# Performance work log

Hardware: AMD Instinct MI355X
Metric: run time of the kernel (lower is better)

Reference implementation:

```python
import jax, jax.numpy as jnp
import numpy as np

DEPTH = 4
CHUNK = 16


def tp(a, b):
    """Graded tensor (outer) product on flattened levels: (...,m)x(...,n)->(...,m*n)."""
    return jnp.einsum('...i,...j->...ij', a, b).reshape(*a.shape[:-1], a.shape[-1] * b.shape[-1])


def ta_mul(a, b):
    """Truncated tensor-algebra product of two group-like elements (implicit level-0 == 1).
    a, b: lists of levels 1..D, level k flattened to C**k."""
    out = []
    for k in range(len(a)):
        t = a[k] + b[k]
        for i in range(k):
            t = t + tp(a[i], b[k - 1 - i])
        out.append(t)
    return out


def ta_mulz(a, b):
    """Product when both elements have level-0 == 0."""
    out = []
    for k in range(len(a)):
        t = jnp.zeros_like(a[k])
        for i in range(k):
            t = t + tp(a[i], b[k - 1 - i])
        out.append(t)
    return out


def ta_exp(a):
    """exp of a level-0-free element, truncated at DEPTH; returns levels 1..D (level-0 == 1 implicit)."""
    out = list(a)
    p = a
    fact = 1.0
    for m in range(2, len(a) + 1):
        p = ta_mulz(a, p)
        fact *= m
        out = [o + q / fact for o, q in zip(out, p)]
    return out


def ta_log(s):
    """Truncated log of group-like element g = 1 + s; input s = levels 1..D of g."""
    out = list(s)
    p = s
    sign = 1.0
    for m in range(2, len(s) + 1):
        p = ta_mulz(s, p)
        sign = -sign
        out = [o + (sign / m) * q for o, q in zip(out, p)]
    return out


def bch(a, b):
    """BCH merge: log(exp(a) (x) exp(b)) in the truncated algebra."""
    return ta_log(ta_mul(ta_exp(a), ta_exp(b)))


def exp_l1(d):
    """exp of a pure level-1 element d (shape (...,C)): level k = d^(x)k / k!."""
    levels = [d]
    cur = d
    fact = 1.0
    for k in range(2, DEPTH + 1):
        cur = tp(cur, d)
        fact *= k
        levels.append(cur / fact)
    return levels


def chunk_signatures(inc):
    """inc: (B, N, L, C) per-chunk increments -> signature levels [(B,N,C), (B,N,C^2), ...]
    via Chen: sig = exp(d_1) (x) ... (x) exp(d_L)."""
    carry0 = tuple(exp_l1(inc[:, :, 0]))
    xs = jnp.moveaxis(inc[:, :, 1:], 2, 0)  # (L-1, B, N, C)
    def step(carry, d):
        return tuple(ta_mul(list(carry), exp_l1(d))), None
    carry, _ = jax.lax.scan(step, carry0, xs)
    return list(carry)


def hillis_steele(levels):
    """Inclusive associative scan over chunk dim (axis=1) with BCH merge.
    bch(0, b) == b exactly, so zero-padding handles the boundary."""
    N = levels[0].shape[1]
    pref = levels
    d = 1
    while d < N:
        shifted = [jnp.concatenate([jnp.zeros_like(l[:, :d]), l[:, :-d]], axis=1) for l in pref]
        pref = bch(shifted, pref)
        d *= 2
    return pref


def _forward(x, W1, b1, W2, b2):
    B, T, Cin = x.shape
    t = jnp.linspace(0.0, 1.0, T, dtype=x.dtype)
    path = jnp.concatenate([x, jnp.broadcast_to(t[None, :, None], (B, T, 1)).astype(x.dtype)], axis=-1)
    C = Cin + 1
    # basepoint=True: path starts at 0, so increments are diff of [0; path]
    inc = jnp.diff(path, axis=1, prepend=jnp.zeros((B, 1, C), x.dtype))
    N = T // CHUNK
    inc = inc.reshape(B, N, CHUNK, C)
    sig = chunk_signatures(inc)          # levels 1..D, (B,N,C^k)
    logl = ta_log(sig)                   # truncated log-signature per chunk
    pref = hillis_steele(logl)           # inclusive BCH prefix scan
    flat = jnp.concatenate(pref, axis=-1)  # (B, N, mem_dim)
    pooled = flat.mean(axis=1)           # readout_pool == 'mean'
    h = jnp.maximum(pooled @ W1 + b1, 0.0)
    return h @ W2 + b2


def setup_inputs() -> dict:
    key = jax.random.key(0)
    k0, k1, k2 = jax.random.split(key, 3)
    B, T, Cin = 8, 2048, 7
    mem_dim, H, out_dim = 4680, 256, 1
    x = jax.random.normal(k0, (B, T, Cin), dtype=jnp.float32)
    W1 = jax.random.normal(k1, (mem_dim, H), dtype=jnp.float32) * (1.0 / np.sqrt(mem_dim))
    b1 = jnp.zeros((H,), jnp.float32)
    W2 = jax.random.normal(k2, (H, out_dim), dtype=jnp.float32) * (1.0 / np.sqrt(H))
    b2 = jnp.zeros((out_dim,), jnp.float32)
    return {"x": x, "W1": W1, "b1": b1, "W2": W2, "b2": b2}


def reference(x, W1, b1, W2, b2):
    return _forward(x, W1, b1, W2, b2)
```

## Files before the change

### kernel.cpp

```cpp
#include <hip/hip_runtime.h>


#define MEM   4680
#define OFF2  8
#define OFF3  72
#define OFF4  584
#define NCH   128
#define NG    32
#define LCH   4
#define TLEN  2048
#define GSTR  20

__global__ __launch_bounds__(256) void group_sig_kernel(const float* __restrict__ x,
                                                        float* __restrict__ Q) {
    int blk = blockIdx.x;
    int b = blk >> 5, g = blk & 31;
    int tid = threadIdx.x;
    int lane = tid & 63, w = tid >> 6;
    int kq = lane >> 3, lq = lane & 7;

    __shared__ float sInc[64 * 8];
    __shared__ __attribute__((aligned(16))) float sG[512 * GSTR];
    __shared__ float sA[MEM];
    __shared__ float loc3[512];
    __shared__ float loc2[64];
    __shared__ float loc1[8];

    for (int e = tid; e < 64 * 8; e += 256) {
        int s = e >> 3, c = e & 7;
        int t = g * 64 + s;
        float v;
        if (c < 7) {
            float cur  = x[(b * TLEN + t) * 7 + c];
            float prev = (t > 0) ? x[(b * TLEN + t - 1) * 7 + c] : 0.0f;
            v = cur - prev;
        } else {
            v = (t > 0) ? (1.0f / 2047.0f) : 0.0f;
        }
        sInc[e] = v;
    }
    for (int m = tid; m < MEM; m += 256) sA[m] = 0.0f;
    __syncthreads();

    for (int c = 0; c < LCH; c++) {
        const float* dch = &sInc[c * 128];

        int pos1 = tid, pos2 = tid + 256;
        int i1 = pos1 >> 6, j1 = (pos1 >> 3) & 7, k1 = pos1 & 7;
        int i2 = pos2 >> 6;
        float p1a = 0.0f, l2a = 0.0f, l3a = 0.0f;
        float p1b = 0.0f, l2b = 0.0f, l3b = 0.0f;
        float ga[16], gb[16];
#pragma unroll
        for (int t = 0; t < 16; t++) {
            float di1 = dch[t * 8 + i1], di2 = dch[t * 8 + i2];
            float dj = dch[t * 8 + j1], dk = dch[t * 8 + k1];
            ga[t] = l3a + dk * (l2a * 0.5f + dj * (p1a * (1.0f / 6.0f) + di1 * (1.0f / 24.0f)));
            gb[t] = l3b + dk * (l2b * 0.5f + dj * (p1b * (1.0f / 6.0f) + di2 * (1.0f / 24.0f)));
            l3a += dk * (l2a + dj * (p1a * 0.5f + di1 * (1.0f / 6.0f)));
            l3b += dk * (l2b + dj * (p1b * 0.5f + di2 * (1.0f / 6.0f)));
            l2a += p1a * dj + di1 * dj * 0.5f;
            l2b += p1b * dj + di2 * dj * 0.5f;
            p1a += di1;
            p1b += di2;
        }
        {
            float4* gp1 = (float4*)&sG[pos1 * GSTR];
            float4* gp2 = (float4*)&sG[pos2 * GSTR];
            gp1[0] = make_float4(ga[0], ga[1], ga[2], ga[3]);
            gp1[1] = make_float4(ga[4], ga[5], ga[6], ga[7]);
            gp1[2] = make_float4(ga[8], ga[9], ga[10], ga[11]);
            gp1[3] = make_float4(ga[12], ga[13], ga[14], ga[15]);
            gp2[0] = make_float4(gb[0], gb[1], gb[2], gb[3]);
            gp2[1] = make_float4(gb[4], gb[5], gb[6], gb[7]);
            gp2[2] = make_float4(gb[8], gb[9], gb[10], gb[11]);
            gp2[3] = make_float4(gb[12], gb[13], gb[14], gb[15]);
        }
        loc3[pos1] = l3a;
        loc3[pos2] = l3b;
        if (k1 == 0) { loc2[pos1 >> 3] = l2a; loc2[pos2 >> 3] = l2b; }
        if ((pos1 & 63) == 0) { loc1[i1] = p1a; loc1[i2] = p1b; }
        __syncthreads();

        float dl[16];
#pragma unroll
        for (int t = 0; t < 16; t++) dl[t] = dch[t * 8 + lq];

        float r4[16];
#pragma unroll
        for (int r = 0; r < 16; r++) {
            int row = w + 4 * r;
            int i = row >> 3, j = row & 7;
            int m = row * 64 + lane;
            const float4* gp = (const float4*)&sG[(row * 8 + kq) * GSTR];
            float4 g0 = gp[0], g1 = gp[1], g2 = gp[2], g3 = gp[3];
            float acc = g0.x * dl[0] + g0.y * dl[1] + g0.z * dl[2] + g0.w * dl[3]
                      + g1.x * dl[4] + g1.y * dl[5] + g1.z * dl[6] + g1.w * dl[7]
                      + g2.x * dl[8] + g2.y * dl[9] + g2.z * dl[10] + g2.w * dl[11]
                      + g3.x * dl[12] + g3.y * dl[13] + g3.z * dl[14] + g3.w * dl[15];
            r4[r] = sA[OFF4 + m] + acc
                  + sA[i] * loc3[j * 64 + lane]
                  + sA[OFF2 + row] * loc2[lane]
                  + sA[OFF3 + row * 8 + kq] * loc1[lq];
        }
        float r3[2];
#pragma unroll
        for (int q = 0; q < 2; q++) {
            int m3 = tid + 256 * q;
            float l3v = (q == 0) ? l3a : l3b;
            r3[q] = sA[OFF3 + m3] + l3v
                  + sA[m3 >> 6] * loc2[m3 & 63]
                  + sA[OFF2 + (m3 >> 3)] * loc1[m3 & 7];
        }
        float r2v = 0.0f, r1v = 0.0f;
        if (tid < 64) r2v = sA[OFF2 + tid] + loc2[tid] + sA[tid >> 3] * loc1[tid & 7];
        if (tid < 8)  r1v = sA[tid] + loc1[tid];
        __syncthreads();

        size_t qbase = (size_t)(blk * LCH + c) * MEM;
#pragma unroll
        for (int r = 0; r < 16; r++) {
            int row = w + 4 * r;
            int m = row * 64 + lane;
            sA[OFF4 + m] = r4[r];
            Q[qbase + OFF4 + m] = r4[r];
        }
        sA[OFF3 + tid] = r3[0];       Q[qbase + OFF3 + tid] = r3[0];
        sA[OFF3 + 256 + tid] = r3[1]; Q[qbase + OFF3 + 256 + tid] = r3[1];
        if (tid < 64) { sA[OFF2 + tid] = r2v; Q[qbase + OFF2 + tid] = r2v; }
        if (tid < 8)  { sA[tid] = r1v;        Q[qbase + tid] = r1v; }
        __syncthreads();
    }
}

__global__ __launch_bounds__(256) void scan_low_kernel(const float* __restrict__ Q,
                                                       float* __restrict__ P) {
    int b = blockIdx.x;
    int tid = threadIdx.x;

    __shared__ float st1[NG][8];
    __shared__ float sp1[NG][8];
    __shared__ float st2[NG][64];
    __shared__ float sp2[NG][64];

    {
        int g = tid >> 3, i = tid & 7;
        st1[g][i] = Q[((size_t)((b * NG + g) * LCH + 3)) * MEM + i];
    }
    for (int m = tid; m < NG * 64; m += 256) {
        int g = m >> 6, e = m & 63;
        st2[g][e] = Q[((size_t)((b * NG + g) * LCH + 3)) * MEM + OFF2 + e];
    }
    __syncthreads();

    if (tid < 8) {
        float acc = 0.0f;
        for (int g = 0; g < NG; g++) { sp1[g][tid] = acc; acc += st1[g][tid]; }
    }
    __syncthreads();
    if (tid < 64) {
        int i = tid >> 3, k = tid & 7;
        float acc = 0.0f;
        for (int g = 0; g < NG; g++) {
            sp2[g][tid] = acc;
            acc += st2[g][tid] + sp1[g][i] * st1[g][k];
        }
    }
    __syncthreads();

    {
        int g = tid >> 3, i = tid & 7;
        P[(size_t)(b * NG + g) * MEM + i] = sp1[g][i];
    }
    for (int m = tid; m < NG * 64; m += 256) {
        int g = m >> 6, e = m & 63;
        P[(size_t)(b * NG + g) * MEM + OFF2 + e] = sp2[g][e];
    }

    int m1 = tid, m2 = tid + 256;
    int i1 = m1 >> 6, jk1 = m1 & 63, ij1 = m1 >> 3, k1 = m1 & 7;
    int i2 = m2 >> 6, jk2 = m2 & 63, ij2 = m2 >> 3, k2 = m2 & 7;
    float acc1 = 0.0f, acc2 = 0.0f;
#pragma unroll 4
    for (int g = 0; g < NG; g++) {
        size_t prow = (size_t)(b * NG + g) * MEM;
        size_t qrow = (size_t)((b * NG + g) * LCH + 3) * MEM;
        P[prow + OFF3 + m1] = acc1;
        P[prow + OFF3 + m2] = acc2;
        acc1 += Q[qrow + OFF3 + m1] + sp1[g][i1] * st2[g][jk1] + sp2[g][ij1] * st1[g][k1];
        acc2 += Q[qrow + OFF3 + m2] + sp1[g][i2] * st2[g][jk2] + sp2[g][ij2] * st1[g][k2];
    }
}

__global__ __launch_bounds__(256) void scan_l4_kernel(const float* __restrict__ Q,
                                                      float* __restrict__ P) {
    int bx = blockIdx.x;
    int b = bx >> 4, s = bx & 15;
    int m = s * 256 + threadIdx.x;
    int i = m >> 9, jkl = m & 511, ij = m >> 6, ijk = m >> 3, kl = m & 63, l = m & 7;

    float acc = 0.0f;
#pragma unroll 4
    for (int g = 0; g < NG; g++) {
        size_t prow = (size_t)(b * NG + g) * MEM;
        size_t qrow = (size_t)((b * NG + g) * LCH + 3) * MEM;
        P[prow + OFF4 + m] = acc;
        acc += Q[qrow + OFF4 + m]
             + P[prow + i] * Q[qrow + OFF3 + jkl]
             + P[prow + OFF2 + ij] * Q[qrow + OFF2 + kl]
             + P[prow + OFF3 + ijk] * Q[qrow + l];
    }
}

__global__ __launch_bounds__(256) void apply_log_pool_kernel(const float* __restrict__ Q,
                                                             const float* __restrict__ P,
                                                             float* __restrict__ pooled) {
    int blk = blockIdx.x;
    int b = blk >> 5;
    int tid = threadIdx.x;
    int lane = tid & 63, w = tid >> 6;
    int kq = lane >> 3, lq = lane & 7;

    __shared__ float sA[MEM];
    __shared__ float sB[MEM];
    __shared__ float sR[OFF4];
    __shared__ float sP23[512];

    {
        size_t pbase = (size_t)blk * MEM;
        const float4* src = (const float4*)(P + pbase);
        float4* dst = (float4*)sA;
        for (int m = tid; m < MEM / 4; m += 256) dst[m] = src[m];
    }

    float pool4[16];
#pragma unroll
    for (int r = 0; r < 16; r++) pool4[r] = 0.0f;
    float pool3[2] = {0.0f, 0.0f};
    float pool2 = 0.0f, pool1 = 0.0f;

    for (int c = 0; c < LCH; c++) {
        __syncthreads();
        {
            size_t baseQ = (size_t)(blk * LCH + c) * MEM;
            const float4* src = (const float4*)(Q + baseQ);
            float4* dst = (float4*)sB;
            for (int m = tid; m < MEM / 4; m += 256) dst[m] = src[m];
        }
        __syncthreads();

        float b1l = sB[lq];
        float b2lane = sB[OFF2 + lane];

        float r1 = 0.0f, r2v = 0.0f;
        float r3v[2];
#pragma unroll
        for (int q = 0; q < 2; q++) {
            int m3 = tid + 256 * q;
            r3v[q] = sA[OFF3 + m3] + sB[OFF3 + m3]
                   + sA[m3 >> 6] * sB[OFF2 + (m3 & 63)]
                   + sA[OFF2 + (m3 >> 3)] * sB[m3 & 7];
        }
        if (tid < 64) r2v = sA[OFF2 + tid] + sB[OFF2 + tid] + sA[tid >> 3] * sB[tid & 7];
        if (tid < 8)  r1 = sA[tid] + sB[tid];

        float r4[16];
#pragma unroll
        for (int r = 0; r < 16; r++) {
            int row = w + 4 * r;
            int i = row >> 3, j = row & 7;
            int m = row * 64 + lane;
            r4[r] = sA[OFF4 + m] + sB[OFF4 + m]
                  + sA[i] * sB[OFF3 + j * 64 + lane]
                  + sA[OFF2 + row] * b2lane
                  + sA[OFF3 + row * 8 + kq] * b1l;
        }

#pragma unroll
        for (int q = 0; q < 2; q++) sR[OFF3 + tid + 256 * q] = r3v[q];
        if (tid < 64) sR[OFF2 + tid] = r2v;
        if (tid < 8)  sR[tid] = r1;
        __syncthreads();

#pragma unroll
        for (int q = 0; q < 2; q++) {
            int m3 = tid + 256 * q;
            int i = m3 >> 6;
            sP23[m3] = sR[i] * sR[OFF2 + (m3 & 63)]
                     + sR[OFF2 + i * 8 + ((m3 >> 3) & 7)] * sR[m3 & 7];
        }
        __syncthreads();

        float s1l = sR[lq];
        float s2lane = sR[OFF2 + lane];
        float p22lane = sR[kq] * sR[lq];
#pragma unroll
        for (int r = 0; r < 16; r++) {
            int row = w + 4 * r;
            int i = row >> 3, j = row & 7;
            float s1i = sR[i];
            float p24 = s1i * sR[OFF3 + j * 64 + lane] + sR[OFF2 + row] * s2lane
                      + sR[OFF3 + row * 8 + kq] * s1l;
            float p34 = s1i * sP23[j * 64 + lane] + sR[OFF2 + row] * p22lane;
            float p44 = s1i * sR[j] * p22lane;
            pool4[r] += r4[r] - 0.5f * p24 + (1.0f / 3.0f) * p34 - 0.25f * p44;
        }
#pragma unroll
        for (int q = 0; q < 2; q++) {
            int m3 = tid + 256 * q;
            int i3 = m3 >> 6;
            pool3[q] += r3v[q] - 0.5f * sP23[m3] + (1.0f / 3.0f) * sR[i3] * p22lane;
        }
        if (tid < 64) pool2 += r2v - 0.5f * sR[tid >> 3] * sR[tid & 7];
        if (tid < 8)  pool1 += r1;
    }

    const float sc = 1.0f / (float)NCH;
    float* pb = pooled + (size_t)b * MEM;
#pragma unroll
    for (int r = 0; r < 16; r++) {
        int row = w + 4 * r;
        atomicAdd(&pb[OFF4 + row * 64 + lane], pool4[r] * sc);
    }
    atomicAdd(&pb[OFF3 + tid], pool3[0] * sc);
    atomicAdd(&pb[OFF3 + 256 + tid], pool3[1] * sc);
    if (tid < 64) atomicAdd(&pb[OFF2 + tid], pool2 * sc);
    if (tid < 8)  atomicAdd(&pb[tid], pool1 * sc);
}

#define ZN (8 * MEM + 8 * 256)
__global__ __launch_bounds__(256) void zero_kernel(float* __restrict__ buf) {
    int i = blockIdx.x * 256 + threadIdx.x;
    if (i < ZN) buf[i] = 0.0f;
}

__global__ __launch_bounds__(256) void gemv1_kernel(const float* __restrict__ pooled,
                                                    const float* __restrict__ W1,
                                                    float* __restrict__ hbuf) {
    int kc = blockIdx.x;
    int tid = threadIdx.x;
    int k0 = kc * 32;
    __shared__ float sp[8][32];
    {
        int b = tid >> 5, kk = tid & 31;
        sp[b][kk] = (k0 + kk < MEM) ? pooled[b * MEM + k0 + kk] : 0.0f;
    }
    __syncthreads();
    float acc[8];
#pragma unroll
    for (int b = 0; b < 8; b++) acc[b] = 0.0f;
    int kend = (k0 + 32 < MEM) ? (k0 + 32) : MEM;
    for (int k = k0; k < kend; k++) {
        float wv = W1[(size_t)k * 256 + tid];
#pragma unroll
        for (int b = 0; b < 8; b++) acc[b] += sp[b][k - k0] * wv;
    }
#pragma unroll
    for (int b = 0; b < 8; b++) atomicAdd(&hbuf[b * 256 + tid], acc[b]);
}

__global__ __launch_bounds__(256) void final_kernel(const float* __restrict__ hbuf,
                                                    const float* __restrict__ b1,
                                                    const float* __restrict__ W2,
                                                    const float* __restrict__ b2,
                                                    float* __restrict__ outp) {
    int b = blockIdx.x;
    int tid = threadIdx.x;
    float v = hbuf[b * 256 + tid] + b1[tid];
    v = fmaxf(v, 0.0f) * W2[tid];
    __shared__ float sRed[256];
    sRed[tid] = v;
    __syncthreads();
    for (int s = 128; s > 0; s >>= 1) {
        if (tid < s) sRed[tid] += sRed[tid + s];
        __syncthreads();
    }
    if (tid == 0) outp[b] = sRed[0] + b2[0];
}

extern "C" void kernel_launch(void* const* d_in, const int* in_sizes, int n_in,
                              void* d_out, int out_size, void* d_ws, size_t ws_size,
                              hipStream_t stream) {
    const float* x  = (const float*)d_in[0];
    const float* W1 = (const float*)d_in[1];
    const float* b1 = (const float*)d_in[2];
    const float* W2 = (const float*)d_in[3];
    const float* b2 = (const float*)d_in[4];
    float* out = (float*)d_out;

    float* ws = (float*)d_ws;
    float* Q      = ws;
    float* P      = Q + (size_t)1024 * MEM;
    float* pooled = P + (size_t)256 * MEM;
    float* hbuf   = pooled + 8 * MEM;

    zero_kernel<<<(ZN + 255) / 256, 256, 0, stream>>>(pooled);
    group_sig_kernel<<<256, 256, 0, stream>>>(x, Q);
    scan_low_kernel<<<8, 256, 0, stream>>>(Q, P);
    scan_l4_kernel<<<128, 256, 0, stream>>>(Q, P);
    apply_log_pool_kernel<<<256, 256, 0, stream>>>(Q, P, pooled);
    gemv1_kernel<<<147, 256, 0, stream>>>(pooled, W1, hbuf);
    final_kernel<<<8, 256, 0, stream>>>(hbuf, b1, W2, b2, out);
}
```

Baseline: 136.6 us.

## Fuse scan kernels, fold zeroing into group kernel, preload all chunks

Merges the low-level and level-4 prefix-scan kernels into one 128-block kernel. Each block recomputes the level-1/2 scans, computes its own slice of level-3, and keeps these prefixes in shared memory so the level-4 pass needs no global P reads. The zero kernel is folded into the group-signature kernel. The apply kernel now loads all four chunk Q rows into shared memory up front, which removes per-chunk syncs but makes shared memory much larger and lowers occupancy. Together these cut two kernel launches and a global round trip of prefix data.

```diff
diff --git a/kernel.cpp b/kernel.cpp
--- a/kernel.cpp
+++ b/kernel.cpp
@@ -10,14 +10,18 @@
 #define LCH   4
 #define TLEN  2048
 #define GSTR  20
+#define ZN    (8 * MEM + 8 * 256)
 
 __global__ __launch_bounds__(256) void group_sig_kernel(const float* __restrict__ x,
-                                                        float* __restrict__ Q) {
+                                                        float* __restrict__ Q,
+                                                        float* __restrict__ zbuf) {
     int blk = blockIdx.x;
     int b = blk >> 5, g = blk & 31;
     int tid = threadIdx.x;
     int lane = tid & 63, w = tid >> 6;
     int kq = lane >> 3, lq = lane & 7;
+
+    for (int i = blk * 256 + tid; i < ZN; i += 256 * 256) zbuf[i] = 0.0f;
 
     __shared__ float sInc[64 * 8];
     __shared__ __attribute__((aligned(16))) float sG[512 * GSTR];
@@ -133,15 +137,18 @@
     }
 }
 
-__global__ __launch_bounds__(256) void scan_low_kernel(const float* __restrict__ Q,
-                                                       float* __restrict__ P) {
-    int b = blockIdx.x;
+__global__ __launch_bounds__(256) void scan_fused_kernel(const float* __restrict__ Q,
+                                                         float* __restrict__ P) {
+    int bx = blockIdx.x;
+    int b = bx >> 4, s = bx & 15;
     int tid = threadIdx.x;
 
     __shared__ float st1[NG][8];
+    __shared__ float st2[NG][64];
+    __shared__ float st3[NG][32];
     __shared__ float sp1[NG][8];
-    __shared__ float st2[NG][64];
     __shared__ float sp2[NG][64];
+    __shared__ float sp3[NG][32];
 
     {
         int g = tid >> 3, i = tid & 7;
@@ -151,64 +158,53 @@
         int g = m >> 6, e = m & 63;
         st2[g][e] = Q[((size_t)((b * NG + g) * LCH + 3)) * MEM + OFF2 + e];
     }
-    __syncthreads();
-
-    if (tid < 8) {
-        float acc = 0.0f;
-        for (int g = 0; g < NG; g++) { sp1[g][tid] = acc; acc += st1[g][tid]; }
-    }
-    __syncthreads();
+    for (int m = tid; m < NG * 32; m += 256) {
+        int g = m >> 5, e = m & 31;
+        st3[g][e] = Q[((size_t)((b * NG + g) * LCH + 3)) * MEM + OFF3 + s * 32 + e];
+    }
+    __syncthreads();
+
     if (tid < 64) {
         int i = tid >> 3, k = tid & 7;
-        float acc = 0.0f;
+        float p1acc = 0.0f, p2acc = 0.0f;
         for (int g = 0; g < NG; g++) {
-            sp2[g][tid] = acc;
-            acc += st2[g][tid] + sp1[g][i] * st1[g][k];
-        }
-    }
-    __syncthreads();
-
-    {
-        int g = tid >> 3, i = tid & 7;
-        P[(size_t)(b * NG + g) * MEM + i] = sp1[g][i];
-    }
-    for (int m = tid; m < NG * 64; m += 256) {
-        int g = m >> 6, e = m & 63;
-        P[(size_t)(b * NG + g) * MEM + OFF2 + e] = sp2[g][e];
-    }
-
-    int m1 = tid, m2 = tid + 256;
-    int i1 = m1 >> 6, jk1 = m1 & 63, ij1 = m1 >> 3, k1 = m1 & 7;
-    int i2 = m2 >> 6, jk2 = m2 & 63, ij2 = m2 >> 3, k2 = m2 & 7;
-    float acc1 = 0.0f, acc2 = 0.0f;
+            sp2[g][tid] = p2acc;
+            if (k == 0) sp1[g][i] = p1acc;
+            if (s == 0) {
+                size_t prow = (size_t)(b * NG + g) * MEM;
+                P[prow + OFF2 + tid] = p2acc;
+                if (k == 0) P[prow + i] = p1acc;
+            }
+            p2acc += st2[g][tid] + p1acc * st1[g][k];
+            p1acc += st1[g][i];
+        }
+    }
+    __syncthreads();
+
+    if (tid < 32) {
+        int ijk = s * 32 + tid;
+        int i = ijk >> 6, jk = ijk & 63, ij = ijk >> 3, k = ijk & 7;
+        float acc3 = 0.0f;
+        for (int g = 0; g < NG; g++) {
+            sp3[g][tid] = acc3;
+            P[(size_t)(b * NG + g) * MEM + OFF3 + ijk] = acc3;
+            acc3 += st3[g][tid] + sp1[g][i] * st2[g][jk] + sp2[g][ij] * st1[g][k];
+        }
+    }
+    __syncthreads();
+
+    int m = s * 256 + tid;
+    int i = m >> 9, jkl = m & 511, ij = m >> 6, ijk_l = tid >> 3, kl = m & 63, l = m & 7;
+    float acc4 = 0.0f;
 #pragma unroll 4
     for (int g = 0; g < NG; g++) {
         size_t prow = (size_t)(b * NG + g) * MEM;
         size_t qrow = (size_t)((b * NG + g) * LCH + 3) * MEM;
-        P[prow + OFF3 + m1] = acc1;
-        P[prow + OFF3 + m2] = acc2;
-        acc1 += Q[qrow + OFF3 + m1] + sp1[g][i1] * st2[g][jk1] + sp2[g][ij1] * st1[g][k1];
-        acc2 += Q[qrow + OFF3 + m2] + sp1[g][i2] * st2[g][jk2] + sp2[g][ij2] * st1[g][k2];
-    }
-}
-
-__global__ __launch_bounds__(256) void scan_l4_kernel(const float* __restrict__ Q,
-                                                      float* __restrict__ P) {
-    int bx = blockIdx.x;
-    int b = bx >> 4, s = bx & 15;
-    int m = s * 256 + threadIdx.x;
-    int i = m >> 9, jkl = m & 511, ij = m >> 6, ijk = m >> 3, kl = m & 63, l = m & 7;
-
-    float acc = 0.0f;
-#pragma unroll 4
-    for (int g = 0; g < NG; g++) {
-        size_t prow = (size_t)(b * NG + g) * MEM;
-        size_t qrow = (size_t)((b * NG + g) * LCH + 3) * MEM;
-        P[prow + OFF4 + m] = acc;
-        acc += Q[qrow + OFF4 + m]
-             + P[prow + i] * Q[qrow + OFF3 + jkl]
-             + P[prow + OFF2 + ij] * Q[qrow + OFF2 + kl]
-             + P[prow + OFF3 + ijk] * Q[qrow + l];
+        P[prow + OFF4 + m] = acc4;
+        acc4 += Q[qrow + OFF4 + m]
+              + sp1[g][i] * Q[qrow + OFF3 + jkl]
+              + sp2[g][ij] * st2[g][kl]
+              + sp3[g][ijk_l] * st1[g][l];
     }
 }
 
@@ -222,16 +218,19 @@
     int kq = lane >> 3, lq = lane & 7;
 
     __shared__ float sA[MEM];
-    __shared__ float sB[MEM];
+    __shared__ float sB[LCH * MEM];
     __shared__ float sR[OFF4];
     __shared__ float sP23[512];
 
     {
-        size_t pbase = (size_t)blk * MEM;
-        const float4* src = (const float4*)(P + pbase);
-        float4* dst = (float4*)sA;
-        for (int m = tid; m < MEM / 4; m += 256) dst[m] = src[m];
-    }
+        const float4* srcP = (const float4*)(P + (size_t)blk * MEM);
+        float4* dstA = (float4*)sA;
+        for (int m = tid; m < MEM / 4; m += 256) dstA[m] = srcP[m];
+        const float4* srcQ = (const float4*)(Q + (size_t)blk * LCH * MEM);
+        float4* dstB = (float4*)sB;
+        for (int m = tid; m < LCH * MEM / 4; m += 256) dstB[m] = srcQ[m];
+    }
+    __syncthreads();
 
     float pool4[16];
 #pragma unroll
@@ -240,29 +239,21 @@
     float pool2 = 0.0f, pool1 = 0.0f;
 
     for (int c = 0; c < LCH; c++) {
-        __syncthreads();
-        {
-            size_t baseQ = (size_t)(blk * LCH + c) * MEM;
-            const float4* src = (const float4*)(Q + baseQ);
-            float4* dst = (float4*)sB;
-            for (int m = tid; m < MEM / 4; m += 256) dst[m] = src[m];
-        }
-        __syncthreads();
-
-        float b1l = sB[lq];
-        float b2lane = sB[OFF2 + lane];
+        const float* sBc = &sB[c * MEM];
+        float b1l = sBc[lq];
+        float b2lane = sBc[OFF2 + lane];
 
         float r1 = 0.0f, r2v = 0.0f;
         float r3v[2];
 #pragma unroll
         for (int q = 0; q < 2; q++) {
             int m3 = tid + 256 * q;
-            r3v[q] = sA[OFF3 + m3] + sB[OFF3 + m3]
-                   + sA[m3 >> 6] * sB[OFF2 + (m3 & 63)]
-                   + sA[OFF2 + (m3 >> 3)] * sB[m3 & 7];
-        }
-        if (tid < 64) r2v = sA[OFF2 + tid] + sB[OFF2 + tid] + sA[tid >> 3] * sB[tid & 7];
-        if (tid < 8)  r1 = sA[tid] + sB[tid];
+            r3v[q] = sA[OFF3 + m3] + sBc[OFF3 + m3]
+                   + sA[m3 >> 6] * sBc[OFF2 + (m3 & 63)]
+                   + sA[OFF2 + (m3 >> 3)] * sBc[m3 & 7];
+        }
+        if (tid < 64) r2v = sA[OFF2 + tid] + sBc[OFF2 + tid] + sA[tid >> 3] * sBc[tid & 7];
+        if (tid < 8)  r1 = sA[tid] + sBc[tid];
 
         float r4[16];
 #pragma unroll
@@ -270,12 +261,13 @@
             int row = w + 4 * r;
             int i = row >> 3, j = row & 7;
             int m = row * 64 + lane;
-            r4[r] = sA[OFF4 + m] + sB[OFF4 + m]
-                  + sA[i] * sB[OFF3 + j * 64 + lane]
+            r4[r] = sA[OFF4 + m] + sBc[OFF4 + m]
+                  + sA[i] * sBc[OFF3 + j * 64 + lane]
                   + sA[OFF2 + row] * b2lane
                   + sA[OFF3 + row * 8 + kq] * b1l;
         }
 
+        __syncthreads();
 #pragma unroll
         for (int q = 0; q < 2; q++) sR[OFF3 + tid + 256 * q] = r3v[q];
         if (tid < 64) sR[OFF2 + tid] = r2v;
@@ -328,12 +320,6 @@
     if (tid < 8)  atomicAdd(&pb[tid], pool1 * sc);
 }
 
-#define ZN (8 * MEM + 8 * 256)
-__global__ __launch_bounds__(256) void zero_kernel(float* __restrict__ buf) {
-    int i = blockIdx.x * 256 + threadIdx.x;
-    if (i < ZN) buf[i] = 0.0f;
-}
-
 __global__ __launch_bounds__(256) void gemv1_kernel(const float* __restrict__ pooled,
                                                     const float* __restrict__ W1,
                                                     float* __restrict__ hbuf) {
@@ -394,10 +380,8 @@
     float* pooled = P + (size_t)256 * MEM;
     float* hbuf   = pooled + 8 * MEM;
 
-    zero_kernel<<<(ZN + 255) / 256, 256, 0, stream>>>(pooled);
-    group_sig_kernel<<<256, 256, 0, stream>>>(x, Q);
-    scan_low_kernel<<<8, 256, 0, stream>>>(Q, P);
-    scan_l4_kernel<<<128, 256, 0, stream>>>(Q, P);
+    group_sig_kernel<<<256, 256, 0, stream>>>(x, Q, pooled);
+    scan_fused_kernel<<<128, 256, 0, stream>>>(Q, P);
     apply_log_pool_kernel<<<256, 256, 0, stream>>>(Q, P, pooled);
     gemv1_kernel<<<147, 256, 0, stream>>>(pooled, W1, hbuf);
     final_kernel<<<8, 256, 0, stream>>>(hbuf, b1, W2, b2, out);
```

Result: faster. 127.5 us (-6.6%).
